# Kernel tuning notes

Hardware: AMD Instinct MI355X
Metric: run time of the kernel (lower is better)

The kernel has to match this reference:

```python
import jax, jax.numpy as jnp
import numpy as np

ALPHA = 0.2  # LeakyReLU negative slope
NEG = -1e12


def setup_inputs() -> dict:
    key = jax.random.key(0)
    ks = jax.random.split(key, 7)
    B, N, Cin, F, H = 4, 2048, 256, 64, 4
    x = jax.random.normal(ks[0], (B, N, Cin), dtype=jnp.float32)
    adj = jax.random.randint(ks[1], (N, N), 0, 2, dtype=jnp.int32)
    W = jax.random.normal(ks[2], (H, Cin, F), dtype=jnp.float32) * (1.414 / np.sqrt(Cin))
    a1 = jax.random.normal(ks[3], (H, F), dtype=jnp.float32) * 0.1
    a2 = jax.random.normal(ks[4], (H, F), dtype=jnp.float32) * 0.1
    Wl = jax.random.normal(ks[5], (F, H * F), dtype=jnp.float32) * (1.0 / np.sqrt(H * F))
    bl = jax.random.normal(ks[6], (F,), dtype=jnp.float32) * 0.01
    return {"x": x, "adj": adj, "W": W, "a1": a1, "a2": a2, "Wl": Wl, "bl": bl}


def leaky(v):
    return jnp.where(v >= 0, v, ALPHA * v)


def reference(x, adj, W, a1, a2, Wl, bl):
    # Eval mode: dropout is a no-op.
    # h: [B,H,N,F] per-head projected features
    h = jnp.einsum("bnc,hcf->bhnf", x, W)
    # additive attention: e[b,h,i,j] = leaky(h_i . a1 + h_j . a2)
    f1 = jnp.einsum("bhnf,hf->bhn", h, a1)  # source term
    f2 = jnp.einsum("bhnf,hf->bhn", h, a2)  # target term
    e = leaky(f1[:, :, :, None] + f2[:, :, None, :])  # [B,H,N,N]
    e = jnp.where(adj[None, None] > 0, e, NEG)
    # NOTE: original softmaxes over dim=1 of [B,N,N], i.e. the i axis (axis=2 here)
    att = jax.nn.softmax(e, axis=2)
    hp = jnp.einsum("bhij,bhjf->bhif", att, h)  # [B,H,N,F]
    hp = jax.nn.relu(hp)  # concat=True heads
    B, H, N, F = hp.shape
    cat = hp.transpose(0, 2, 1, 3).reshape(B, N, H * F)
    out = leaky(cat @ Wl.T + bl)  # n_heads > 1 -> linear + leakyrelu
    return out
```

## Files before the change

kernel.cpp:

```cpp
#include <hip/hip_runtime.h>
#include <hip/hip_bf16.h>
#include <stdint.h>

typedef __attribute__((ext_vector_type(8))) short short8;
typedef __attribute__((ext_vector_type(4))) float f32x4;
typedef _Float16 f16;
typedef __attribute__((ext_vector_type(8))) f16 f16x8;
typedef __attribute__((ext_vector_type(2))) f16 f16x2;
typedef uint32_t u32;
typedef uint16_t u16;
typedef uint8_t u8;

#define LOG2E 1.4426950408889634f


__device__ __forceinline__ u16 f2bf(float f){
  union{float f; u32 u;} x; x.f = f;
  u32 r = x.u + 0x7FFFu + ((x.u >> 16) & 1u);
  return (u16)(r >> 16);
}
__device__ __forceinline__ u32 pkbf(float a, float b){
  __hip_bfloat162 h = __float22bfloat162_rn(float2{a, b});
  union{ __hip_bfloat162 h; u32 u; } cv; cv.h = h;
  return cv.u;
}
__device__ __forceinline__ u32 pkh(float a, float b){
  f16x2 h; h.x = (f16)a; h.y = (f16)b;
  union{ f16x2 h; u32 u; } cv; cv.h = h;
  return cv.u;
}
__device__ __forceinline__ f16x2 uh2(u32 x){ union{u32 u; f16x2 h;} v; v.u = x; return v.h; }
__device__ __forceinline__ u32 h2u(f16x2 x){ union{f16x2 h; u32 u;} v; v.h = x; return v.u; }

__global__ __launch_bounds__(256) void k_front(const float* __restrict__ x,
      const float* __restrict__ W, const float* __restrict__ a1, const float* __restrict__ a2,
      const int* __restrict__ adj,
      u8* __restrict__ adjb, u16* __restrict__ hT,
      float* __restrict__ Aarr, float* __restrict__ Barr,
      float* __restrict__ Cexp, float* __restrict__ Dexp,
      float* __restrict__ Dsum){
  int bid = blockIdx.x, t = threadIdx.x;

  if (bid >= 2560){
    Dsum[(bid - 2560)*256 + t] = 0.f;
    return;
  }
  if (bid >= 512){
    int idx = (bid - 512)*256 + t;
    const int4* ap = (const int4*)(adj + (size_t)idx*8);
    int4 v0 = ap[0], v1 = ap[1];
    u32 byte = (u32)(v0.x > 0)        | ((u32)(v0.y > 0) << 1)
             | ((u32)(v0.z > 0) << 2) | ((u32)(v0.w > 0) << 3)
             | ((u32)(v1.x > 0) << 4) | ((u32)(v1.y > 0) << 5)
             | ((u32)(v1.z > 0) << 6) | ((u32)(v1.w > 0) << 7);
    adjb[idx] = (u8)byte;
    return;
  }
  __shared__ u16 WL[64*264];
  int xcd = bid & 7, slot = bid >> 3;
  int rt = xcd*16 + (slot & 15);
  int cb = slot >> 4;
  const float* Wh = W + (size_t)cb*16384;
  {
    int f0 = (t & 15)*4;
    int cg = t >> 4;
    int s = ((f0 >> 2) & 7) << 3;
    #pragma unroll
    for (int it2 = 0; it2 < 4; it2++){
      int c0 = (cg + it2*16)*4;
      float4 wv0 = *(const float4*)(Wh + (size_t)(c0+0)*64 + f0);
      float4 wv1 = *(const float4*)(Wh + (size_t)(c0+1)*64 + f0);
      float4 wv2 = *(const float4*)(Wh + (size_t)(c0+2)*64 + f0);
      float4 wv3 = *(const float4*)(Wh + (size_t)(c0+3)*64 + f0);
      int cc = c0 ^ s;
      #pragma unroll
      for (int k = 0; k < 4; k++){
        u32 lo = pkbf((&wv0.x)[k], (&wv1.x)[k]);
        u32 hi = pkbf((&wv2.x)[k], (&wv3.x)[k]);
        *(uint2*)&WL[(f0+k)*264 + cc] = uint2{lo, hi};
      }
    }
  }
  __syncthreads();

  int w = t >> 6, l = t & 63;
  int rA = rt*64 + w*16 + (l & 15);
  int kg = (l >> 4) * 8;
  int rowq[4], rswq[4];
  #pragma unroll
  for (int q = 0; q < 4; q++){
    rowq[q] = q*16 + (l & 15);
    rswq[q] = ((rowq[q] >> 2) & 7) << 3;
  }
  f32x4 acc[4] = {};
  const float* xrow = x + (size_t)rA * 256;
  #pragma unroll
  for (int ks = 0; ks < 8; ks++){
    int c = ks*32 + kg;
    float4 xa = *(const float4*)(xrow + c);
    float4 xb = *(const float4*)(xrow + c + 4);
    union{u32 w[4]; short8 v;} A;
    A.w[0] = pkbf(xa.x, xa.y); A.w[1] = pkbf(xa.z, xa.w);
    A.w[2] = pkbf(xb.x, xb.y); A.w[3] = pkbf(xb.z, xb.w);
    #pragma unroll
    for (int q = 0; q < 4; q++){
      short8 Bf = *(const short8*)&WL[rowq[q]*264 + (c ^ rswq[q])];
      acc[q] = __builtin_amdgcn_mfma_f32_16x16x32_bf16(A.v, Bf, acc[q], 0, 0, 0);
    }
  }
  int rb = rt*64 + w*16 + (l >> 4)*4;
  int b = rb >> 11, n = rb & 2047;
  #pragma unroll
  for (int q = 0; q < 4; q++){
    int f = q*16 + (l & 15);
    u32 p0 = pkh(acc[q][0], acc[q][1]);
    u32 p1 = pkh(acc[q][2], acc[q][3]);
    u16* dst = hT + ((size_t)(b*4 + cb)*64 + f)*2048 + n;
    *(uint2*)dst = uint2{p0, p1};
  }
  float a1v[4], a2v[4];
  #pragma unroll
  for (int q = 0; q < 4; q++){
    a1v[q] = a1[cb*64 + q*16 + (l & 15)];
    a2v[q] = a2[cb*64 + q*16 + (l & 15)];
  }
  float s1[4], s2[4];
  #pragma unroll
  for (int r = 0; r < 4; r++){
    s1[r] = acc[0][r]*a1v[0] + acc[1][r]*a1v[1] + acc[2][r]*a1v[2] + acc[3][r]*a1v[3];
    s2[r] = acc[0][r]*a2v[0] + acc[1][r]*a2v[1] + acc[2][r]*a2v[2] + acc[3][r]*a2v[3];
  }
  #pragma unroll
  for (int m = 1; m <= 8; m <<= 1){
    #pragma unroll
    for (int r = 0; r < 4; r++){
      s1[r] += __shfl_xor(s1[r], m);
      s2[r] += __shfl_xor(s2[r], m);
    }
  }
  if ((l & 15) == 0){
    #pragma unroll
    for (int r = 0; r < 4; r++){
      int row = rb + r;
      int bb = row >> 11, nn = row & 2047;
      int o = (bb*4 + cb)*2048 + nn;
      float fa = s1[r] * LOG2E;
      Aarr[o] = __builtin_amdgcn_exp2f(fa);
      Barr[o] = __builtin_amdgcn_exp2f(0.2f*fa);
      float fb = s2[r] * LOG2E;
      Cexp[o] = __builtin_amdgcn_exp2f(fb);
      Dexp[o] = __builtin_amdgcn_exp2f(0.2f*fb);
    }
  }
}

__global__ __launch_bounds__(256) void k_colsum(const u32* __restrict__ adjw,
      const float* __restrict__ Aarr, const float* __restrict__ Barr,
      const float* __restrict__ Cexp, const float* __restrict__ Dexp,
      float* __restrict__ Dsum){
  __shared__ float AL[128*16], BL[128*16];
  __shared__ float red[4][1024];
  int jt = blockIdx.x;
  int is = blockIdx.y;
  int t = threadIdx.x, w = t >> 6, l = t & 63;
  int i0 = is*128;
  for (int k = t; k < 2048; k += 256){
    int bh = k >> 7, ii = k & 127;
    AL[ii*16 + bh] = Aarr[bh*2048 + i0 + ii];
    BL[ii*16 + bh] = Barr[bh*2048 + i0 + ii];
  }
  int j = jt*64 + l;
  float Cj[16], Dj[16];
  #pragma unroll
  for (int bh = 0; bh < 16; bh++){
    Cj[bh] = Cexp[bh*2048 + j];
    Dj[bh] = Dexp[bh*2048 + j];
  }
  float acc[16] = {};
  __syncthreads();
  int wi = jt*2 + (l >> 5), sh = l & 31;
  const u32* aw = adjw + wi;
  #pragma unroll 2
  for (int ii = w*32; ii < w*32 + 32; ii++){
    u32 m = aw[(size_t)(i0 + ii)*64];
    float bitf = (float)((m >> sh) & 1u);
    const float* ar = &AL[ii*16];
    const float* br = &BL[ii*16];
    #pragma unroll
    for (int q = 0; q < 4; q++){
      float4 a4 = *(const float4*)(ar + q*4);
      float4 b4 = *(const float4*)(br + q*4);
      acc[q*4+0] = fmaf(fmaxf(a4.x*Cj[q*4+0], b4.x*Dj[q*4+0]), bitf, acc[q*4+0]);
      acc[q*4+1] = fmaf(fmaxf(a4.y*Cj[q*4+1], b4.y*Dj[q*4+1]), bitf, acc[q*4+1]);
      acc[q*4+2] = fmaf(fmaxf(a4.z*Cj[q*4+2], b4.z*Dj[q*4+2]), bitf, acc[q*4+2]);
      acc[q*4+3] = fmaf(fmaxf(a4.w*Cj[q*4+3], b4.w*Dj[q*4+3]), bitf, acc[q*4+3]);
    }
  }
  #pragma unroll
  for (int bh = 0; bh < 16; bh++) red[w][bh*64 + l] = acc[bh];
  __syncthreads();
  #pragma unroll
  for (int k = 0; k < 4; k++){
    int e = t*4 + k;
    float s = (red[0][e] + red[1][e]) + (red[2][e] + red[3][e]);
    int bh = e >> 6, jl = e & 63;
    atomicAdd(&Dsum[bh*2048 + jt*64 + jl], s);
  }
}

__global__ __launch_bounds__(256) void k_pv(const u32* __restrict__ adjw, const u16* __restrict__ hT,
      const float* __restrict__ Aarr, const float* __restrict__ Barr,
      const float* __restrict__ Cexp, const float* __restrict__ Dexp,
      const float* __restrict__ Dsum, u16* __restrict__ part){
  int hw = blockIdx.x;
  int work = (hw & 7)*64 + (hw >> 3);
  int bh = work >> 5;
  int jh = (work >> 4) & 1;
  int it = work & 15;
  int b = bh >> 2, h = bh & 3;
  int t = threadIdx.x;
  int w = t >> 6, l = t & 63;

  __shared__ u16 hTl[2][64*136];
  __shared__ u32 CA2l[512];
  __shared__ u32 DB2l[512];

  {
    int gj = bh*2048 + jh*1024 + t*4;
    float4 c4 = *(const float4*)(Cexp + gj);
    float4 d4 = *(const float4*)(Dexp + gj);
    float4 s4 = *(const float4*)(Dsum + gj);
    float i0v = 16.0f/s4.x, i1v = 16.0f/s4.y, i2v = 16.0f/s4.z, i3v = 16.0f/s4.w;
    CA2l[t*2]   = pkh(c4.x*i0v, c4.y*i1v);
    CA2l[t*2+1] = pkh(c4.z*i2v, c4.w*i3v);
    DB2l[t*2]   = pkh(d4.x*i0v, d4.y*i1v);
    DB2l[t*2+1] = pkh(d4.z*i2v, d4.w*i3v);
  }

  int i0 = it*128 + w*32 + (l & 15);
  f16x2 Ai02, Bi02, Ai12, Bi12;
  {
    const float sc = 0.0625f;
    float A0 = Aarr[bh*2048 + i0] * sc,      B0 = Barr[bh*2048 + i0] * sc;
    float A1 = Aarr[bh*2048 + i0 + 16] * sc, B1 = Barr[bh*2048 + i0 + 16] * sc;
    Ai02 = uh2(pkh(A0, A0)); Bi02 = uh2(pkh(B0, B0));
    Ai12 = uh2(pkh(A1, A1)); Bi12 = uh2(pkh(B1, B1));
  }
  const u16* hTr = hT + (size_t)bh * 64 * 2048;
  int kg = (l >> 4) * 8;
  f32x4 acc[2][4] = {};

  int sf = t >> 2, sseg = (t & 3) * 32;
  const u16* srcbase = hTr + (size_t)sf*2048 + sseg + jh*1024;
  uint4 r0, r1, r2, r3;
  {
    const u16* src = srcbase;
    r0 = *(const uint4*)(src);      r1 = *(const uint4*)(src + 8);
    r2 = *(const uint4*)(src + 16); r3 = *(const uint4*)(src + 24);
    u16* d = &hTl[0][sf*136 + sseg];
    *(uint4*)(d) = r0; *(uint4*)(d + 8) = r1; *(uint4*)(d + 16) = r2; *(uint4*)(d + 24) = r3;
  }
  int cur = 0;

  for (int jj = 0; jj < 1024; jj += 128){
    int jc = jh*1024 + jj;
    __syncthreads();
    bool more = (jj + 128) < 1024;
    if (more){
      const u16* src = srcbase + jj + 128;
      r0 = *(const uint4*)(src);      r1 = *(const uint4*)(src + 8);
      r2 = *(const uint4*)(src + 16); r3 = *(const uint4*)(src + 24);
    }
    uint4 mw0 = *(const uint4*)(adjw + (size_t)i0*64 + (jc >> 5));
    uint4 mw1 = *(const uint4*)(adjw + (size_t)(i0+16)*64 + (jc >> 5));
    const u16* hbuf = hTl[cur];
    #pragma unroll
    for (int ks = 0; ks < 4; ks++){
      int pbase = (jj >> 1) + ks*16 + (l >> 4)*4;
      uint4 ca2 = *(const uint4*)&CA2l[pbase];
      uint4 db2 = *(const uint4*)&DB2l[pbase];
      u32 w0 = (&mw0.x)[ks] >> kg;
      u32 w1 = (&mw1.x)[ks] >> kg;
      union{u32 w[4]; f16x8 v;} A0u, A1u;
      #pragma unroll
      for (int p = 0; p < 4; p++){
        f16x2 cav = uh2((&ca2.x)[p]);
        f16x2 dbv = uh2((&db2.x)[p]);
        f16x2 e0 = __builtin_elementwise_max(Ai02*cav, Bi02*dbv);
        f16x2 e1 = __builtin_elementwise_max(Ai12*cav, Bi12*dbv);
        u32 m0 = ((u32)((int)(w0 << (31-2*p)) >> 31) & 0x0000FFFFu)
               | ((u32)((int)(w0 << (30-2*p)) >> 31) & 0xFFFF0000u);
        u32 m1 = ((u32)((int)(w1 << (31-2*p)) >> 31) & 0x0000FFFFu)
               | ((u32)((int)(w1 << (30-2*p)) >> 31) & 0xFFFF0000u);
        A0u.w[p] = h2u(e0) & m0;
        A1u.w[p] = h2u(e1) & m1;
      }
      #pragma unroll
      for (int q = 0; q < 4; q++){
        f16x8 Bf = *(const f16x8*)&hbuf[(q*16 + (l & 15))*136 + ks*32 + kg];
        acc[0][q] = __builtin_amdgcn_mfma_f32_16x16x32_f16(A0u.v, Bf, acc[0][q], 0, 0, 0);
        acc[1][q] = __builtin_amdgcn_mfma_f32_16x16x32_f16(A1u.v, Bf, acc[1][q], 0, 0, 0);
      }
    }
    if (more){
      u16* d = &hTl[cur ^ 1][sf*136 + sseg];
      *(uint4*)(d) = r0; *(uint4*)(d + 8) = r1; *(uint4*)(d + 16) = r2; *(uint4*)(d + 24) = r3;
      cur ^= 1;
    }
  }
  u16* pr = part + ((size_t)(jh*4 + b)*2048)*256;
  #pragma unroll
  for (int r = 0; r < 2; r++){
    int nb = it*128 + w*32 + r*16 + (l >> 4)*4;
    #pragma unroll
    for (int q = 0; q < 4; q++){
      int f = h*64 + q*16 + (l & 15);
      #pragma unroll
      for (int rr = 0; rr < 4; rr++){
        pr[(size_t)(nb + rr)*256 + f] = f2bf(acc[r][q][rr]);
      }
    }
  }
}

__global__ __launch_bounds__(128) void k_out(const u16* __restrict__ part,
                       const float* __restrict__ Wl, const float* __restrict__ bl,
                       float* __restrict__ out){
  int rt = blockIdx.x;
  int w = threadIdx.x >> 6, l = threadIdx.x & 63;
  int rA = rt*32 + w*16 + (l & 15);
  int b = rA >> 11, n = rA & 2047;
  const u16* p0 = part + ((size_t)b*2048 + n)*256;
  const u16* p1 = part + ((size_t)(4 + b)*2048 + n)*256;
  int kg = (l >> 4) * 8;
  f32x4 acc[4] = {};
  #pragma unroll
  for (int ks = 0; ks < 8; ks++){
    int c = ks*32 + kg;
    short8 v0 = *(const short8*)(p0 + c);
    short8 v1 = *(const short8*)(p1 + c);
    float av[8];
    #pragma unroll
    for (int e = 0; e < 8; e++){
      union{u32 u; float f;} x0, x1;
      x0.u = ((u32)(u16)v0[e]) << 16;
      x1.u = ((u32)(u16)v1[e]) << 16;
      av[e] = fmaxf(x0.f + x1.f, 0.f);
    }
    union{u32 w[4]; short8 v;} A;
    A.w[0] = pkbf(av[0], av[1]); A.w[1] = pkbf(av[2], av[3]);
    A.w[2] = pkbf(av[4], av[5]); A.w[3] = pkbf(av[6], av[7]);
    #pragma unroll
    for (int q = 0; q < 4; q++){
      const float* wr = Wl + (size_t)(q*16 + (l & 15))*256 + c;
      float4 u0 = *(const float4*)(wr);
      float4 u1 = *(const float4*)(wr + 4);
      union{u32 w[4]; short8 v;} Bv;
      Bv.w[0] = pkbf(u0.x, u0.y); Bv.w[1] = pkbf(u0.z, u0.w);
      Bv.w[2] = pkbf(u1.x, u1.y); Bv.w[3] = pkbf(u1.z, u1.w);
      acc[q] = __builtin_amdgcn_mfma_f32_16x16x32_bf16(A.v, Bv.v, acc[q], 0, 0, 0);
    }
  }
  int rb = rt*32 + w*16 + (l >> 4)*4;
  #pragma unroll
  for (int q = 0; q < 4; q++){
    int o = q*16 + (l & 15);
    float bv = bl[o];
    #pragma unroll
    for (int r = 0; r < 4; r++){
      float v = acc[q][r] + bv;
      out[(size_t)(rb + r)*64 + o] = fmaxf(v, 0.2f*v);
    }
  }
}

extern "C" void kernel_launch(void* const* d_in, const int* in_sizes, int n_in,
                              void* d_out, int out_size, void* d_ws, size_t ws_size,
                              hipStream_t stream) {
  const float* x  = (const float*)d_in[0];
  const int* adj  = (const int*)d_in[1];
  const float* W  = (const float*)d_in[2];
  const float* a1 = (const float*)d_in[3];
  const float* a2 = (const float*)d_in[4];
  const float* Wl = (const float*)d_in[5];
  const float* bl = (const float*)d_in[6];
  float* out = (float*)d_out;
  char* ws = (char*)d_ws;

  u32* adjw    = (u32*)(ws + 0x0000000);
  u16* hT      = (u16*)(ws + 0x0080000);
  u16* part    = (u16*)(ws + 0x0480000);
  float* Aarr  = (float*)(ws + 0x1480000);
  float* Barr  = (float*)(ws + 0x14A0000);
  float* Cexp  = (float*)(ws + 0x14C0000);
  float* Dexp  = (float*)(ws + 0x14E0000);
  float* Dsum  = (float*)(ws + 0x1500000);

  k_front<<<2688, 256, 0, stream>>>(x, W, a1, a2, adj, (u8*)adjw, hT, Aarr, Barr, Cexp, Dexp, Dsum);
  k_colsum<<<dim3(32, 16), 256, 0, stream>>>(adjw, Aarr, Barr, Cexp, Dexp, Dsum);
  k_pv<<<512, 256, 0, stream>>>(adjw, hT, Aarr, Barr, Cexp, Dexp, Dsum, part);
  k_out<<<256, 128, 0, stream>>>(part, Wl, bl, out);
}
```

Baseline: 69.01 us.

## Fuse output projection into k_pv via last-block atomic counter

```diff
diff --git a/kernel.cpp b/kernel.cpp
--- a/kernel.cpp
+++ b/kernel.cpp
@@ -38,9 +38,13 @@
       u8* __restrict__ adjb, u16* __restrict__ hT,
       float* __restrict__ Aarr, float* __restrict__ Barr,
       float* __restrict__ Cexp, float* __restrict__ Dexp,
-      float* __restrict__ Dsum){
+      float* __restrict__ Dsum, u32* __restrict__ cnt){
   int bid = blockIdx.x, t = threadIdx.x;
 
+  if (bid >= 2688){
+    if (t < 64) cnt[t] = 0;
+    return;
+  }
   if (bid >= 2560){
     Dsum[(bid - 2560)*256 + t] = 0.f;
     return;
@@ -211,7 +215,9 @@
 __global__ __launch_bounds__(256) void k_pv(const u32* __restrict__ adjw, const u16* __restrict__ hT,
       const float* __restrict__ Aarr, const float* __restrict__ Barr,
       const float* __restrict__ Cexp, const float* __restrict__ Dexp,
-      const float* __restrict__ Dsum, u16* __restrict__ part){
+      const float* __restrict__ Dsum, u16* __restrict__ part,
+      const float* __restrict__ Wl, const float* __restrict__ bl,
+      float* __restrict__ out, u32* __restrict__ cnt){
   int hw = blockIdx.x;
   int work = (hw & 7)*64 + (hw >> 3);
   int bh = work >> 5;
@@ -224,6 +230,7 @@
   __shared__ u16 hTl[2][64*136];
   __shared__ u32 CA2l[512];
   __shared__ u32 DB2l[512];
+  __shared__ int oldflag;
 
   {
     int gj = bh*2048 + jh*1024 + t*4;
@@ -295,12 +302,14 @@
         A0u.w[p] = h2u(e0) & m0;
         A1u.w[p] = h2u(e1) & m1;
       }
+      __builtin_amdgcn_s_setprio(1);
       #pragma unroll
       for (int q = 0; q < 4; q++){
         f16x8 Bf = *(const f16x8*)&hbuf[(q*16 + (l & 15))*136 + ks*32 + kg];
         acc[0][q] = __builtin_amdgcn_mfma_f32_16x16x32_f16(A0u.v, Bf, acc[0][q], 0, 0, 0);
         acc[1][q] = __builtin_amdgcn_mfma_f32_16x16x32_f16(A1u.v, Bf, acc[1][q], 0, 0, 0);
       }
+      __builtin_amdgcn_s_setprio(0);
     }
     if (more){
       u16* d = &hTl[cur ^ 1][sf*136 + sseg];
@@ -321,55 +330,65 @@
       }
     }
   }
-}
-
-__global__ __launch_bounds__(128) void k_out(const u16* __restrict__ part,
-                       const float* __restrict__ Wl, const float* __restrict__ bl,
-                       float* __restrict__ out){
-  int rt = blockIdx.x;
-  int w = threadIdx.x >> 6, l = threadIdx.x & 63;
-  int rA = rt*32 + w*16 + (l & 15);
-  int b = rA >> 11, n = rA & 2047;
-  const u16* p0 = part + ((size_t)b*2048 + n)*256;
-  const u16* p1 = part + ((size_t)(4 + b)*2048 + n)*256;
-  int kg = (l >> 4) * 8;
-  f32x4 acc[4] = {};
-  #pragma unroll
-  for (int ks = 0; ks < 8; ks++){
-    int c = ks*32 + kg;
-    short8 v0 = *(const short8*)(p0 + c);
-    short8 v1 = *(const short8*)(p1 + c);
-    float av[8];
-    #pragma unroll
-    for (int e = 0; e < 8; e++){
-      union{u32 u; float f;} x0, x1;
-      x0.u = ((u32)(u16)v0[e]) << 16;
-      x1.u = ((u32)(u16)v1[e]) << 16;
-      av[e] = fmaxf(x0.f + x1.f, 0.f);
-    }
-    union{u32 w[4]; short8 v;} A;
-    A.w[0] = pkbf(av[0], av[1]); A.w[1] = pkbf(av[2], av[3]);
-    A.w[2] = pkbf(av[4], av[5]); A.w[3] = pkbf(av[6], av[7]);
-    #pragma unroll
-    for (int q = 0; q < 4; q++){
-      const float* wr = Wl + (size_t)(q*16 + (l & 15))*256 + c;
-      float4 u0 = *(const float4*)(wr);
-      float4 u1 = *(const float4*)(wr + 4);
-      union{u32 w[4]; short8 v;} Bv;
-      Bv.w[0] = pkbf(u0.x, u0.y); Bv.w[1] = pkbf(u0.z, u0.w);
-      Bv.w[2] = pkbf(u1.x, u1.y); Bv.w[3] = pkbf(u1.z, u1.w);
-      acc[q] = __builtin_amdgcn_mfma_f32_16x16x32_bf16(A.v, Bv.v, acc[q], 0, 0, 0);
-    }
-  }
-  int rb = rt*32 + w*16 + (l >> 4)*4;
-  #pragma unroll
-  for (int q = 0; q < 4; q++){
-    int o = q*16 + (l & 15);
-    float bv = bl[o];
-    #pragma unroll
-    for (int r = 0; r < 4; r++){
-      float v = acc[q][r] + bv;
-      out[(size_t)(rb + r)*64 + o] = fmaxf(v, 0.2f*v);
+
+  __threadfence();
+  __syncthreads();
+  if (t == 0) oldflag = (int)atomicAdd(&cnt[b*16 + it], 1u);
+  __syncthreads();
+  if (oldflag == 7){
+    __threadfence();
+    int n0 = it*128;
+    const u16* pa = part + ((size_t)b*2048 + n0)*256;
+    const u16* pb = part + ((size_t)(4 + b)*2048 + n0)*256;
+    int rowb = w*32 + (l & 15);
+    f32x4 oacc[2][4] = {};
+    #pragma unroll
+    for (int ks = 0; ks < 8; ks++){
+      int c = ks*32 + kg;
+      union{u32 w[4]; short8 v;} A0, A1;
+      #pragma unroll
+      for (int r2 = 0; r2 < 2; r2++){
+        const u16* q0 = pa + (size_t)(rowb + r2*16)*256 + c;
+        const u16* q1 = pb + (size_t)(rowb + r2*16)*256 + c;
+        short8 v0 = *(const short8*)(q0);
+        short8 v1 = *(const short8*)(q1);
+        float av[8];
+        #pragma unroll
+        for (int e = 0; e < 8; e++){
+          union{u32 u; float f;} x0, x1;
+          x0.u = ((u32)(u16)v0[e]) << 16;
+          x1.u = ((u32)(u16)v1[e]) << 16;
+          av[e] = fmaxf(x0.f + x1.f, 0.f);
+        }
+        u32* Aw = r2 ? A1.w : A0.w;
+        Aw[0] = pkbf(av[0], av[1]); Aw[1] = pkbf(av[2], av[3]);
+        Aw[2] = pkbf(av[4], av[5]); Aw[3] = pkbf(av[6], av[7]);
+      }
+      #pragma unroll
+      for (int q = 0; q < 4; q++){
+        const float* wr = Wl + (size_t)(q*16 + (l & 15))*256 + c;
+        float4 u0 = *(const float4*)(wr);
+        float4 u1 = *(const float4*)(wr + 4);
+        union{u32 w[4]; short8 v;} Bv;
+        Bv.w[0] = pkbf(u0.x, u0.y); Bv.w[1] = pkbf(u0.z, u0.w);
+        Bv.w[2] = pkbf(u1.x, u1.y); Bv.w[3] = pkbf(u1.z, u1.w);
+        oacc[0][q] = __builtin_amdgcn_mfma_f32_16x16x32_bf16(A0.v, Bv.v, oacc[0][q], 0, 0, 0);
+        oacc[1][q] = __builtin_amdgcn_mfma_f32_16x16x32_bf16(A1.v, Bv.v, oacc[1][q], 0, 0, 0);
+      }
+    }
+    #pragma unroll
+    for (int r2 = 0; r2 < 2; r2++){
+      int rb2 = b*2048 + n0 + w*32 + r2*16 + (l >> 4)*4;
+      #pragma unroll
+      for (int q = 0; q < 4; q++){
+        int o = q*16 + (l & 15);
+        float bv = bl[o];
+        #pragma unroll
+        for (int r = 0; r < 4; r++){
+          float v = oacc[r2][q][r] + bv;
+          out[(size_t)(rb2 + r)*64 + o] = fmaxf(v, 0.2f*v);
+        }
+      }
     }
   }
 }
@@ -395,9 +414,9 @@
   float* Cexp  = (float*)(ws + 0x14C0000);
   float* Dexp  = (float*)(ws + 0x14E0000);
   float* Dsum  = (float*)(ws + 0x1500000);
-
-  k_front<<<2688, 256, 0, stream>>>(x, W, a1, a2, adj, (u8*)adjw, hT, Aarr, Barr, Cexp, Dexp, Dsum);
+  u32* cnt     = (u32*)(ws + 0x1520000);
+
+  k_front<<<2689, 256, 0, stream>>>(x, W, a1, a2, adj, (u8*)adjw, hT, Aarr, Barr, Cexp, Dexp, Dsum, cnt);
   k_colsum<<<dim3(32, 16), 256, 0, stream>>>(adjw, Aarr, Barr, Cexp, Dexp, Dsum);
-  k_pv<<<512, 256, 0, stream>>>(adjw, hT, Aarr, Barr, Cexp, Dexp, Dsum, part);
-  k_out<<<256, 128, 0, stream>>>(part, Wl, bl, out);
-}
+  k_pv<<<512, 256, 0, stream>>>(adjw, hT, Aarr, Barr, Cexp, Dexp, Dsum, part, Wl, bl, out, cnt);
+}
```

New measurement: 134.4 us. 1.95x slower.
